# Performance work log

Hardware: AMD Instinct MI355X
Metric: run time of the kernel (lower is better)

## Reference

```python
import jax, jax.numpy as jnp
import numpy as np

EPS = 1e-5

def _layernorm(x, g, b):
    mu = jnp.mean(x, axis=-1, keepdims=True)
    var = jnp.mean(jnp.square(x - mu), axis=-1, keepdims=True)
    return (x - mu) * jax.lax.rsqrt(var + EPS) * g + b

def setup_inputs() -> dict:
    S, B, D, H, F = 4096, 2, 512, 8, 2048
    key = jax.random.key(0)
    ks = jax.random.split(key, 10)
    sc = 0.02
    return {
        "src": jax.random.normal(ks[0], (S, B, D), jnp.float32),
        "qkv_w": jax.random.normal(ks[1], (3 * D, D), jnp.float32) * sc,
        "qkv_b": jnp.zeros((3 * D,), jnp.float32),
        "out_w": jax.random.normal(ks[2], (D, D), jnp.float32) * sc,
        "w1": jax.random.normal(ks[3], (F, D), jnp.float32) * sc,
        "b1": jnp.zeros((F,), jnp.float32),
        "w2": jax.random.normal(ks[4], (D, F), jnp.float32) * sc,
        "b2": jnp.zeros((D,), jnp.float32),
        "ln1_g": jnp.ones((D,), jnp.float32),
        "ln1_b": jnp.zeros((D,), jnp.float32),
        "ln2_g": jnp.ones((D,), jnp.float32),
        "ln2_b": jnp.zeros((D,), jnp.float32),
    }

def reference(src, qkv_w, qkv_b, out_w, w1, b1, w2, b2, ln1_g, ln1_b, ln2_g, ln2_b):
    S, B, D = src.shape
    H = 8
    hd = D // H
    # --- self attention (NOTE: no 1/sqrt(hd) scaling, matching source) ---
    qkv = src @ qkv_w.T + qkv_b                      # [S, B, 3D]
    q, k, v = jnp.split(qkv, 3, axis=-1)             # each [S, B, D]
    # [S, B*H, hd] -> [B*H, S, hd]
    q = q.reshape(S, B * H, hd).transpose(1, 0, 2)
    k = k.reshape(S, B * H, hd).transpose(1, 0, 2)
    v = v.reshape(S, B * H, hd).transpose(1, 0, 2)
    scores = jnp.einsum('nqd,nkd->nqk', q, k)        # [B*H, S, S]
    attn = jax.nn.softmax(scores, axis=-1)           # dropout = identity (eval)
    out = jnp.einsum('nqk,nkd->nqd', attn, v)        # [B*H, S, hd]
    out = out.transpose(1, 0, 2).reshape(S, B, D)
    attn_out = out @ out_w.T                         # out_proj has no bias
    # --- post-norm residual + FFN ---
    x = _layernorm(src + attn_out, ln1_g, ln1_b)
    ffn = jax.nn.relu(x @ w1.T + b1) @ w2.T + b2
    x = _layernorm(x + ffn, ln2_g, ln2_b)
    return x
```

## Files before the change

### kernel.cpp

```cpp
#include <hip/hip_runtime.h>
#include <cstdint>
#include <math.h>

#define CF4(p) (*reinterpret_cast<const float4*>(p))
#define F4(p)  (*reinterpret_cast<float4*>(p))

typedef __attribute__((ext_vector_type(8))) short bf16x8;
typedef __attribute__((ext_vector_type(4))) float f32x4;

__device__ __forceinline__ unsigned short f2bf(float x) {
  union { float f; unsigned int u; } v; v.f = x;
  unsigned int r = v.u + 0x7FFF + ((v.u >> 16) & 1);
  return (unsigned short)(r >> 16);
}

__device__ __forceinline__ int swz(int row, int col) {
  return row * 64 + (col ^ ((row & 7) << 3));
}

__device__ __forceinline__ void gload_lds16(const void* g, void* lds) {
  __builtin_amdgcn_global_load_lds(
      (const __attribute__((address_space(1))) void*)g,
      (__attribute__((address_space(3))) void*)lds, 16, 0, 0);
}

__global__ __launch_bounds__(256) void cvt_kernel(
    unsigned short* __restrict__ dst, const float* __restrict__ s, int n8)
{
  const int i = blockIdx.x * 256 + threadIdx.x;
  if (i >= n8) return;
  float4 a = CF4(&s[i * 8]), b = CF4(&s[i * 8 + 4]);
  union { bf16x8 v; unsigned short u[8]; } w;
  w.u[0] = f2bf(a.x); w.u[1] = f2bf(a.y); w.u[2] = f2bf(a.z); w.u[3] = f2bf(a.w);
  w.u[4] = f2bf(b.x); w.u[5] = f2bf(b.y); w.u[6] = f2bf(b.z); w.u[7] = f2bf(b.w);
  *reinterpret_cast<bf16x8*>(&dst[i * 8]) = w.v;
}

template<int BIAS, int RELU, int RES, int OBF>
__global__ __launch_bounds__(256, 2) void bgemm_kernel(
    void* __restrict__ Cv, const unsigned short* __restrict__ A,
    const unsigned short* __restrict__ W, const float* __restrict__ bias,
    const float* __restrict__ R, int M, int N, int K)
{
  __shared__ __align__(16) unsigned short As[2][128 * 64];
  __shared__ __align__(16) unsigned short Ws[2][128 * 64];

  const int t    = threadIdx.x;
  const int lane = t & 63, wid = t >> 6;
  const int g    = lane >> 4, lr = lane & 15;
  const int wm   = wid >> 1,  wn = wid & 1;
  const int m0   = blockIdx.y * 128, n0 = blockIdx.x * 128;

  const int sr8 = lane >> 3;
  const int sc  = (lane & 7) ^ sr8;
  const unsigned short* Ag = A + (size_t)(m0 + sr8) * K + sc * 8;
  const unsigned short* Wg = W + (size_t)(n0 + sr8) * K + sc * 8;

  f32x4 acc[4][4];
#pragma unroll
  for (int mi = 0; mi < 4; ++mi)
#pragma unroll
    for (int nj = 0; nj < 4; ++nj)
      acc[mi][nj] = (f32x4){0.f, 0.f, 0.f, 0.f};

#define STAGE_G(buf, k0)                                              \
  {                                                                   \
    _Pragma("unroll")                                                 \
    for (int i = 0; i < 4; ++i) {                                     \
      const int rb = wid * 32 + i * 8;                                \
      gload_lds16(Ag + (size_t)rb * K + (k0), (void*)&As[buf][rb * 64]); \
      gload_lds16(Wg + (size_t)rb * K + (k0), (void*)&Ws[buf][rb * 64]); \
    }                                                                 \
  }

  STAGE_G(0, 0);
  __syncthreads();

  const int nk = K >> 6;
  for (int kt = 0; kt < nk; ++kt) {
    const int cur = kt & 1;
    if (kt + 1 < nk) STAGE_G(cur ^ 1, (kt + 1) * 64);
#pragma unroll
    for (int ks = 0; ks < 2; ++ks) {
      bf16x8 af[4], bfr[4];
#pragma unroll
      for (int mi = 0; mi < 4; ++mi) {
        const int row = wm * 64 + mi * 16 + lr;
        af[mi] = *reinterpret_cast<const bf16x8*>(
            &As[cur][row * 64 + (((ks * 4 + g) ^ (row & 7)) * 8)]);
      }
#pragma unroll
      for (int nj = 0; nj < 4; ++nj) {
        const int row = wn * 64 + nj * 16 + lr;
        bfr[nj] = *reinterpret_cast<const bf16x8*>(
            &Ws[cur][row * 64 + (((ks * 4 + g) ^ (row & 7)) * 8)]);
      }
#pragma unroll
      for (int mi = 0; mi < 4; ++mi)
#pragma unroll
        for (int nj = 0; nj < 4; ++nj)
          acc[mi][nj] = __builtin_amdgcn_mfma_f32_16x16x32_bf16(
              af[mi], bfr[nj], acc[mi][nj], 0, 0, 0);
    }
    __syncthreads();
  }
#undef STAGE_G

#pragma unroll
  for (int mi = 0; mi < 4; ++mi) {
#pragma unroll
    for (int reg = 0; reg < 4; ++reg) {
      const int r = m0 + wm * 64 + mi * 16 + g * 4 + reg;
#pragma unroll
      for (int nj = 0; nj < 4; ++nj) {
        const int cc = n0 + wn * 64 + nj * 16 + lr;
        float v = acc[mi][nj][reg];
        if (BIAS) v += bias[cc];
        if (RES)  v += R[(size_t)r * N + cc];
        if (RELU) v = fmaxf(v, 0.f);
        if (OBF)  ((unsigned short*)Cv)[(size_t)r * N + cc] = f2bf(v);
        else      ((float*)Cv)[(size_t)r * N + cc] = v;
      }
    }
  }
}

__global__ __launch_bounds__(256, 2) void attn_kernel(
    unsigned short* __restrict__ O, const unsigned short* __restrict__ qkv)
{
  const int Bb = 2, LD = 1536, DM = 512;
  const int qt = blockIdx.x;
  const int nh = blockIdx.y;
  const int b = nh >> 3, h = nh & 7;
  const int cq = h * 64, ck = 512 + h * 64, cv = 1024 + h * 64;

  __shared__ __align__(16) unsigned short Ks [2][64 * 64];
  __shared__ __align__(16) unsigned short Vts[2][64 * 64];
  __shared__ __align__(16) unsigned short Ps [128 * 64];

  const int t    = threadIdx.x;
  const int lane = t & 63;
  const int wid  = t >> 6;
  const int g    = lane >> 4;
  const int lr   = lane & 15;
  const int wq0  = wid * 32;

  bf16x8 qf[2][2];
#pragma unroll
  for (int mi = 0; mi < 2; ++mi)
#pragma unroll
    for (int kq = 0; kq < 2; ++kq)
      qf[mi][kq] = *reinterpret_cast<const bf16x8*>(
          &qkv[((size_t)(qt * 128 + wq0 + mi * 16 + lr) * Bb + b) * LD
               + cq + kq * 32 + g * 8]);

  f32x4 o_acc[2][4];
  float lsum[2] = {0.f, 0.f};
#pragma unroll
  for (int mi = 0; mi < 2; ++mi)
#pragma unroll
    for (int dj = 0; dj < 4; ++dj)
      o_acc[mi][dj] = (f32x4){0.f, 0.f, 0.f, 0.f};

  const int sr8 = lane >> 3;
  const int scK = (lane & 7) ^ sr8;
  const int vD0 = wid * 8;
  const int vSr = lane;

#define STAGE_K(buf, kt)                                               \
  {                                                                    \
    _Pragma("unroll")                                                  \
    for (int i = 0; i < 2; ++i) {                                      \
      const int rb = wid * 16 + i * 8;                                 \
      gload_lds16(&qkv[((size_t)((kt) * 64 + rb + sr8) * Bb + b) * LD  \
                       + ck + scK * 8],                                \
                  (void*)&Ks[buf][rb * 64]);                           \
    }                                                                  \
  }
#define LOAD_V(kt)                                                     \
  {                                                                    \
    _Pragma("unroll")                                                  \
    for (int p = 0; p < 2; ++p)                                        \
      vr[p] = *reinterpret_cast<const bf16x8*>(                        \
          &qkv[((size_t)((kt) * 64 + vSr) * Bb + b) * LD + cv          \
               + vD0 + p * 32]);                                       \
  }
#define WRITE_V(buf)                                                   \
  {                                                                    \
    _Pragma("unroll")                                                  \
    for (int p = 0; p < 2; ++p) {                                      \
      const int d0 = vD0 + p * 32;                                     \
      union { bf16x8 v; unsigned short u[8]; } w;                      \
      w.v = vr[p];                                                     \
      _Pragma("unroll")                                                \
      for (int j = 0; j < 8; ++j)                                      \
        Vts[buf][swz(d0 + j, vSr)] = w.u[j];                           \
    }                                                                  \
  }

  bf16x8 vr[2];
  STAGE_K(0, 0);
  LOAD_V(0);
  WRITE_V(0);
  __syncthreads();

  for (int kt = 0; kt < 64; ++kt) {
    const int cur = kt & 1;
    const bool hasNext = (kt < 63);
    if (hasNext) { STAGE_K(cur ^ 1, kt + 1); LOAD_V(kt + 1); }

    f32x4 sfT[2][4];
#pragma unroll
    for (int mi = 0; mi < 2; ++mi)
#pragma unroll
      for (int nj = 0; nj < 4; ++nj)
        sfT[mi][nj] = (f32x4){0.f, 0.f, 0.f, 0.f};
    __builtin_amdgcn_s_setprio(1);
#pragma unroll
    for (int nj = 0; nj < 4; ++nj) {
#pragma unroll
      for (int kq = 0; kq < 2; ++kq) {
        bf16x8 ak = *reinterpret_cast<const bf16x8*>(
            &Ks[cur][swz(nj * 16 + lr, kq * 32 + g * 8)]);
        sfT[0][nj] = __builtin_amdgcn_mfma_f32_16x16x32_bf16(
            ak, qf[0][kq], sfT[0][nj], 0, 0, 0);
        sfT[1][nj] = __builtin_amdgcn_mfma_f32_16x16x32_bf16(
            ak, qf[1][kq], sfT[1][nj], 0, 0, 0);
      }
    }
    __builtin_amdgcn_s_setprio(0);

#pragma unroll
    for (int mi = 0; mi < 2; ++mi) {
      const int qrow = wq0 + mi * 16 + lr;
#pragma unroll
      for (int nj = 0; nj < 4; ++nj) {
        const float p0 = __expf(sfT[mi][nj][0]);
        const float p1 = __expf(sfT[mi][nj][1]);
        const float p2 = __expf(sfT[mi][nj][2]);
        const float p3 = __expf(sfT[mi][nj][3]);
        lsum[mi] += (p0 + p1) + (p2 + p3);
        unsigned int w0, w1;
        asm("v_cvt_pk_bf16_f32 %0, %1, %2" : "=v"(w0) : "v"(p0), "v"(p1));
        asm("v_cvt_pk_bf16_f32 %0, %1, %2" : "=v"(w1) : "v"(p2), "v"(p3));
        *reinterpret_cast<uint2*>(&Ps[swz(qrow, nj * 16 + g * 4)]) =
            make_uint2(w0, w1);
      }
    }

    __builtin_amdgcn_s_setprio(1);
#pragma unroll
    for (int kks = 0; kks < 2; ++kks) {
      bf16x8 pa0 = *reinterpret_cast<const bf16x8*>(
          &Ps[swz(wq0 +  0 + lr, kks * 32 + g * 8)]);
      bf16x8 pa1 = *reinterpret_cast<const bf16x8*>(
          &Ps[swz(wq0 + 16 + lr, kks * 32 + g * 8)]);
#pragma unroll
      for (int dj = 0; dj < 4; ++dj) {
        bf16x8 vb = *reinterpret_cast<const bf16x8*>(
            &Vts[cur][swz(dj * 16 + lr, kks * 32 + g * 8)]);
        o_acc[0][dj] = __builtin_amdgcn_mfma_f32_16x16x32_bf16(
            pa0, vb, o_acc[0][dj], 0, 0, 0);
        o_acc[1][dj] = __builtin_amdgcn_mfma_f32_16x16x32_bf16(
            pa1, vb, o_acc[1][dj], 0, 0, 0);
      }
    }
    __builtin_amdgcn_s_setprio(0);

    if (hasNext) WRITE_V(cur ^ 1);
    __syncthreads();
  }
#undef STAGE_K
#undef LOAD_V
#undef WRITE_V

#pragma unroll
  for (int mi = 0; mi < 2; ++mi) {
    float rs = lsum[mi];
    rs += __shfl_xor(rs, 16);
    rs += __shfl_xor(rs, 32);
#pragma unroll
    for (int reg = 0; reg < 4; ++reg) {
      const float rsq = __shfl(rs, (lane & 48) + g * 4 + reg);
      const float inv = 1.f / rsq;
      const int q = qt * 128 + wq0 + mi * 16 + g * 4 + reg;
#pragma unroll
      for (int dj = 0; dj < 4; ++dj)
        O[((size_t)q * Bb + b) * DM + h * 64 + dj * 16 + lr] =
            f2bf(o_acc[mi][dj][reg] * inv);
    }
  }
}

template<int WBF>
__global__ __launch_bounds__(256) void ln_kernel(
    float* __restrict__ out, unsigned short* __restrict__ obf,
    const float* __restrict__ in, const float* __restrict__ g,
    const float* __restrict__ bb)
{
  const int w = threadIdx.x >> 6, lane = threadIdx.x & 63;
  const size_t row = (size_t)blockIdx.x * 4 + w;
  const float* xr = in + row * 512;
  float4 v0 = CF4(&xr[lane * 4]);
  float4 v1 = CF4(&xr[256 + lane * 4]);
  float s = v0.x + v0.y + v0.z + v0.w + v1.x + v1.y + v1.z + v1.w;
  float q = v0.x*v0.x + v0.y*v0.y + v0.z*v0.z + v0.w*v0.w
          + v1.x*v1.x + v1.y*v1.y + v1.z*v1.z + v1.w*v1.w;
#pragma unroll
  for (int off = 1; off < 64; off <<= 1) {
    s += __shfl_xor(s, off);
    q += __shfl_xor(q, off);
  }
  const float mu  = s * (1.f / 512.f);
  const float var = q * (1.f / 512.f) - mu * mu;
  const float rst = rsqrtf(var + 1e-5f);
  float4 g0 = CF4(&g[lane * 4]),  g1 = CF4(&g[256 + lane * 4]);
  float4 b0 = CF4(&bb[lane * 4]), b1 = CF4(&bb[256 + lane * 4]);
  float* orow = out + row * 512;
  float4 o0, o1;
  o0.x = (v0.x - mu) * rst * g0.x + b0.x;
  o0.y = (v0.y - mu) * rst * g0.y + b0.y;
  o0.z = (v0.z - mu) * rst * g0.z + b0.z;
  o0.w = (v0.w - mu) * rst * g0.w + b0.w;
  o1.x = (v1.x - mu) * rst * g1.x + b1.x;
  o1.y = (v1.y - mu) * rst * g1.y + b1.y;
  o1.z = (v1.z - mu) * rst * g1.z + b1.z;
  o1.w = (v1.w - mu) * rst * g1.w + b1.w;
  F4(&orow[lane * 4]) = o0;
  F4(&orow[256 + lane * 4]) = o1;
  if (WBF) {
    unsigned short* brow = obf + row * 512;
    ushort4 u0 = make_ushort4(f2bf(o0.x), f2bf(o0.y), f2bf(o0.z), f2bf(o0.w));
    ushort4 u1 = make_ushort4(f2bf(o1.x), f2bf(o1.y), f2bf(o1.z), f2bf(o1.w));
    *reinterpret_cast<ushort4*>(&brow[lane * 4]) = u0;
    *reinterpret_cast<ushort4*>(&brow[256 + lane * 4]) = u1;
  }
}

extern "C" void kernel_launch(void* const* d_in, const int* in_sizes, int n_in,
                              void* d_out, int out_size, void* d_ws, size_t ws_size,
                              hipStream_t stream)
{
  const float* src   = (const float*)d_in[0];
  const float* qkv_w = (const float*)d_in[1];
  const float* qkv_b = (const float*)d_in[2];
  const float* out_w = (const float*)d_in[3];
  const float* w1    = (const float*)d_in[4];
  const float* b1    = (const float*)d_in[5];
  const float* w2    = (const float*)d_in[6];
  const float* b2    = (const float*)d_in[7];
  const float* ln1g  = (const float*)d_in[8];
  const float* ln1b  = (const float*)d_in[9];
  const float* ln2g  = (const float*)d_in[10];
  const float* ln2b  = (const float*)d_in[11];
  float* out = (float*)d_out;

  const int M = 8192;

  char* ws = (char*)d_ws;
  unsigned short* qkv_bf  = (unsigned short*)(ws + 0);
  unsigned short* attn_bf = (unsigned short*)(ws + 25165824);
  unsigned short* h_bf    = (unsigned short*)(ws + 0);
  float*          y       = (float*)(ws + 33554432);
  float*          z       = (float*)(ws + 33554432);
  float*          x       = (float*)(ws + 50331648);
  unsigned short* x_bf    = (unsigned short*)(ws + 67108864);
  unsigned short* src_bf  = (unsigned short*)(ws + 75497472);
  unsigned short* wqkv_bf = (unsigned short*)(ws + 83886080);
  unsigned short* wout_bf = (unsigned short*)(ws + 85458944);
  unsigned short* w1_bf   = (unsigned short*)(ws + 85983232);
  unsigned short* w2_bf   = (unsigned short*)(ws + 88080384);
  if (ws_size < (size_t)90177536) return;

  dim3 blk(256);

  cvt_kernel<<<dim3(2048), blk, 0, stream>>>(src_bf, src, 524288);
  cvt_kernel<<<dim3(384),  blk, 0, stream>>>(wqkv_bf, qkv_w, 98304);
  cvt_kernel<<<dim3(128),  blk, 0, stream>>>(wout_bf, out_w, 32768);
  cvt_kernel<<<dim3(512),  blk, 0, stream>>>(w1_bf, w1, 131072);
  cvt_kernel<<<dim3(512),  blk, 0, stream>>>(w2_bf, w2, 131072);

  bgemm_kernel<1,0,0,1><<<dim3(12, 64), blk, 0, stream>>>(
      qkv_bf, src_bf, wqkv_bf, qkv_b, nullptr, M, 1536, 512);
  attn_kernel<<<dim3(32, 16), blk, 0, stream>>>(attn_bf, qkv_bf);
  bgemm_kernel<0,0,1,0><<<dim3(4, 64), blk, 0, stream>>>(
      y, attn_bf, wout_bf, nullptr, src, M, 512, 512);
  ln_kernel<1><<<dim3(M / 4), blk, 0, stream>>>(x, x_bf, y, ln1g, ln1b);
  bgemm_kernel<1,1,0,1><<<dim3(16, 64), blk, 0, stream>>>(
      h_bf, x_bf, w1_bf, b1, nullptr, M, 2048, 512);
  bgemm_kernel<1,0,1,0><<<dim3(4, 64), blk, 0, stream>>>(
      z, h_bf, w2_bf, b2, x, M, 512, 2048);
  ln_kernel<0><<<dim3(M / 4), blk, 0, stream>>>(out, nullptr, z, ln2g, ln2b);
}
```

Before: 321.7 us.

## Merge weight conversions, narrow N tiles for D=512 GEMMs, enlarge attention blocks

Merges the five fp32-to-bf16 conversion launches into a single kernel. Adds a template parameter for the GEMM N tile and uses 64-wide tiles for the two N=512 GEMMs, doubling their grid to 512 blocks for better CU fill. The attention kernel moves to 512 threads covering 256 queries per block, with K/V staging split over 8 waves so each K/V tile is reused by more queries. Risks: lower per-block arithmetic intensity in the narrow GEMMs, and in attention fewer blocks (256) plus more LDS and register pressure per block.

```diff
diff --git a/kernel.cpp b/kernel.cpp
--- a/kernel.cpp
+++ b/kernel.cpp
@@ -24,53 +24,68 @@
       (__attribute__((address_space(3))) void*)lds, 16, 0, 0);
 }
 
-__global__ __launch_bounds__(256) void cvt_kernel(
-    unsigned short* __restrict__ dst, const float* __restrict__ s, int n8)
-{
-  const int i = blockIdx.x * 256 + threadIdx.x;
-  if (i >= n8) return;
+__global__ __launch_bounds__(256) void cvt_all_kernel(
+    const float* __restrict__ src,   unsigned short* __restrict__ src_bf,
+    const float* __restrict__ qkvw,  unsigned short* __restrict__ qkvw_bf,
+    const float* __restrict__ outw,  unsigned short* __restrict__ outw_bf,
+    const float* __restrict__ w1,    unsigned short* __restrict__ w1_bf,
+    const float* __restrict__ w2,    unsigned short* __restrict__ w2_bf)
+{
+  int i = blockIdx.x * 256 + threadIdx.x;
+  const float* s; unsigned short* d;
+  if      (i < 524288) { s = src;  d = src_bf;                        }
+  else if (i < 622592) { s = qkvw; d = qkvw_bf; i -= 524288;          }
+  else if (i < 655360) { s = outw; d = outw_bf; i -= 622592;          }
+  else if (i < 786432) { s = w1;   d = w1_bf;   i -= 655360;          }
+  else if (i < 917504) { s = w2;   d = w2_bf;   i -= 786432;          }
+  else return;
   float4 a = CF4(&s[i * 8]), b = CF4(&s[i * 8 + 4]);
   union { bf16x8 v; unsigned short u[8]; } w;
   w.u[0] = f2bf(a.x); w.u[1] = f2bf(a.y); w.u[2] = f2bf(a.z); w.u[3] = f2bf(a.w);
   w.u[4] = f2bf(b.x); w.u[5] = f2bf(b.y); w.u[6] = f2bf(b.z); w.u[7] = f2bf(b.w);
-  *reinterpret_cast<bf16x8*>(&dst[i * 8]) = w.v;
-}
-
-template<int BIAS, int RELU, int RES, int OBF>
+  *reinterpret_cast<bf16x8*>(&d[i * 8]) = w.v;
+}
+
+template<int BNT, int BIAS, int RELU, int RES, int OBF>
 __global__ __launch_bounds__(256, 2) void bgemm_kernel(
     void* __restrict__ Cv, const unsigned short* __restrict__ A,
     const unsigned short* __restrict__ W, const float* __restrict__ bias,
     const float* __restrict__ R, int M, int N, int K)
 {
+  constexpr int NJ = BNT / 32;
   __shared__ __align__(16) unsigned short As[2][128 * 64];
-  __shared__ __align__(16) unsigned short Ws[2][128 * 64];
+  __shared__ __align__(16) unsigned short Ws[2][BNT * 64];
 
   const int t    = threadIdx.x;
   const int lane = t & 63, wid = t >> 6;
   const int g    = lane >> 4, lr = lane & 15;
   const int wm   = wid >> 1,  wn = wid & 1;
-  const int m0   = blockIdx.y * 128, n0 = blockIdx.x * 128;
+  const int m0   = blockIdx.y * 128, n0 = blockIdx.x * BNT;
 
   const int sr8 = lane >> 3;
   const int sc  = (lane & 7) ^ sr8;
   const unsigned short* Ag = A + (size_t)(m0 + sr8) * K + sc * 8;
   const unsigned short* Wg = W + (size_t)(n0 + sr8) * K + sc * 8;
 
-  f32x4 acc[4][4];
+  f32x4 acc[4][NJ];
 #pragma unroll
   for (int mi = 0; mi < 4; ++mi)
 #pragma unroll
-    for (int nj = 0; nj < 4; ++nj)
+    for (int nj = 0; nj < NJ; ++nj)
       acc[mi][nj] = (f32x4){0.f, 0.f, 0.f, 0.f};
 
-#define STAGE_G(buf, k0)                                              \
-  {                                                                   \
-    _Pragma("unroll")                                                 \
-    for (int i = 0; i < 4; ++i) {                                     \
-      const int rb = wid * 32 + i * 8;                                \
-      gload_lds16(Ag + (size_t)rb * K + (k0), (void*)&As[buf][rb * 64]); \
-      gload_lds16(Wg + (size_t)rb * K + (k0), (void*)&Ws[buf][rb * 64]); \
-    }                                                                 \
+#define STAGE_G(buf, k0)                                                   \
+  {                                                                        \
+    _Pragma("unroll")                                                      \
+    for (int i = 0; i < 4; ++i) {                                          \
+      const int rb = wid * 32 + i * 8;                                     \
+      gload_lds16(Ag + (size_t)rb * K + (k0), (void*)&As[buf][rb * 64]);   \
+    }                                                                      \
+    _Pragma("unroll")                                                      \
+    for (int i = 0; i < BNT / 32; ++i) {                                   \
+      const int rb = wid * (BNT / 4) + i * 8;                              \
+      gload_lds16(Wg + (size_t)rb * K + (k0), (void*)&Ws[buf][rb * 64]);   \
+    }                                                                      \
   }
 
   STAGE_G(0, 0);
@@ -82,7 +97,7 @@
     if (kt + 1 < nk) STAGE_G(cur ^ 1, (kt + 1) * 64);
 #pragma unroll
     for (int ks = 0; ks < 2; ++ks) {
-      bf16x8 af[4], bfr[4];
+      bf16x8 af[4], bfr[NJ];
 #pragma unroll
       for (int mi = 0; mi < 4; ++mi) {
         const int row = wm * 64 + mi * 16 + lr;
@@ -90,15 +105,15 @@
             &As[cur][row * 64 + (((ks * 4 + g) ^ (row & 7)) * 8)]);
       }
 #pragma unroll
-      for (int nj = 0; nj < 4; ++nj) {
-        const int row = wn * 64 + nj * 16 + lr;
+      for (int nj = 0; nj < NJ; ++nj) {
+        const int row = wn * (BNT / 2) + nj * 16 + lr;
         bfr[nj] = *reinterpret_cast<const bf16x8*>(
             &Ws[cur][row * 64 + (((ks * 4 + g) ^ (row & 7)) * 8)]);
       }
 #pragma unroll
       for (int mi = 0; mi < 4; ++mi)
 #pragma unroll
-        for (int nj = 0; nj < 4; ++nj)
+        for (int nj = 0; nj < NJ; ++nj)
           acc[mi][nj] = __builtin_amdgcn_mfma_f32_16x16x32_bf16(
               af[mi], bfr[nj], acc[mi][nj], 0, 0, 0);
     }
@@ -112,8 +127,8 @@
     for (int reg = 0; reg < 4; ++reg) {
       const int r = m0 + wm * 64 + mi * 16 + g * 4 + reg;
 #pragma unroll
-      for (int nj = 0; nj < 4; ++nj) {
-        const int cc = n0 + wn * 64 + nj * 16 + lr;
+      for (int nj = 0; nj < NJ; ++nj) {
+        const int cc = n0 + wn * (BNT / 2) + nj * 16 + lr;
         float v = acc[mi][nj][reg];
         if (BIAS) v += bias[cc];
         if (RES)  v += R[(size_t)r * N + cc];
@@ -125,7 +140,7 @@
   }
 }
 
-__global__ __launch_bounds__(256, 2) void attn_kernel(
+__global__ __launch_bounds__(512, 2) void attn_kernel(
     unsigned short* __restrict__ O, const unsigned short* __restrict__ qkv)
 {
   const int Bb = 2, LD = 1536, DM = 512;
@@ -136,7 +151,7 @@
 
   __shared__ __align__(16) unsigned short Ks [2][64 * 64];
   __shared__ __align__(16) unsigned short Vts[2][64 * 64];
-  __shared__ __align__(16) unsigned short Ps [128 * 64];
+  __shared__ __align__(16) unsigned short Ps [256 * 64];
 
   const int t    = threadIdx.x;
   const int lane = t & 63;
@@ -151,7 +166,7 @@
 #pragma unroll
     for (int kq = 0; kq < 2; ++kq)
       qf[mi][kq] = *reinterpret_cast<const bf16x8*>(
-          &qkv[((size_t)(qt * 128 + wq0 + mi * 16 + lr) * Bb + b) * LD
+          &qkv[((size_t)(qt * 256 + wq0 + mi * 16 + lr) * Bb + b) * LD
                + cq + kq * 32 + g * 8]);
 
   f32x4 o_acc[2][4];
@@ -169,36 +184,26 @@
 
 #define STAGE_K(buf, kt)                                               \
   {                                                                    \
-    _Pragma("unroll")                                                  \
-    for (int i = 0; i < 2; ++i) {                                      \
-      const int rb = wid * 16 + i * 8;                                 \
-      gload_lds16(&qkv[((size_t)((kt) * 64 + rb + sr8) * Bb + b) * LD  \
-                       + ck + scK * 8],                                \
-                  (void*)&Ks[buf][rb * 64]);                           \
-    }                                                                  \
+    const int rb = wid * 8;                                            \
+    gload_lds16(&qkv[((size_t)((kt) * 64 + rb + sr8) * Bb + b) * LD    \
+                     + ck + scK * 8],                                  \
+                (void*)&Ks[buf][rb * 64]);                             \
   }
 #define LOAD_V(kt)                                                     \
   {                                                                    \
-    _Pragma("unroll")                                                  \
-    for (int p = 0; p < 2; ++p)                                        \
-      vr[p] = *reinterpret_cast<const bf16x8*>(                        \
-          &qkv[((size_t)((kt) * 64 + vSr) * Bb + b) * LD + cv          \
-               + vD0 + p * 32]);                                       \
+    vr = *reinterpret_cast<const bf16x8*>(                             \
+        &qkv[((size_t)((kt) * 64 + vSr) * Bb + b) * LD + cv + vD0]);   \
   }
 #define WRITE_V(buf)                                                   \
   {                                                                    \
+    union { bf16x8 v; unsigned short u[8]; } w;                        \
+    w.v = vr;                                                          \
     _Pragma("unroll")                                                  \
-    for (int p = 0; p < 2; ++p) {                                      \
-      const int d0 = vD0 + p * 32;                                     \
-      union { bf16x8 v; unsigned short u[8]; } w;                      \
-      w.v = vr[p];                                                     \
-      _Pragma("unroll")                                                \
-      for (int j = 0; j < 8; ++j)                                      \
-        Vts[buf][swz(d0 + j, vSr)] = w.u[j];                           \
-    }                                                                  \
-  }
-
-  bf16x8 vr[2];
+    for (int j = 0; j < 8; ++j)                                        \
+      Vts[buf][swz(vD0 + j, vSr)] = w.u[j];                            \
+  }
+
+  bf16x8 vr;
   STAGE_K(0, 0);
   LOAD_V(0);
   WRITE_V(0);
@@ -283,7 +288,7 @@
     for (int reg = 0; reg < 4; ++reg) {
       const float rsq = __shfl(rs, (lane & 48) + g * 4 + reg);
       const float inv = 1.f / rsq;
-      const int q = qt * 128 + wq0 + mi * 16 + g * 4 + reg;
+      const int q = qt * 256 + wq0 + mi * 16 + g * 4 + reg;
 #pragma unroll
       for (int dj = 0; dj < 4; ++dj)
         O[((size_t)q * Bb + b) * DM + h * 64 + dj * 16 + lr] =
@@ -374,21 +379,18 @@
 
   dim3 blk(256);
 
-  cvt_kernel<<<dim3(2048), blk, 0, stream>>>(src_bf, src, 524288);
-  cvt_kernel<<<dim3(384),  blk, 0, stream>>>(wqkv_bf, qkv_w, 98304);
-  cvt_kernel<<<dim3(128),  blk, 0, stream>>>(wout_bf, out_w, 32768);
-  cvt_kernel<<<dim3(512),  blk, 0, stream>>>(w1_bf, w1, 131072);
-  cvt_kernel<<<dim3(512),  blk, 0, stream>>>(w2_bf, w2, 131072);
-
-  bgemm_kernel<1,0,0,1><<<dim3(12, 64), blk, 0, stream>>>(
+  cvt_all_kernel<<<dim3(3584), blk, 0, stream>>>(
+      src, src_bf, qkv_w, wqkv_bf, out_w, wout_bf, w1, w1_bf, w2, w2_bf);
+
+  bgemm_kernel<128,1,0,0,1><<<dim3(12, 64), blk, 0, stream>>>(
       qkv_bf, src_bf, wqkv_bf, qkv_b, nullptr, M, 1536, 512);
-  attn_kernel<<<dim3(32, 16), blk, 0, stream>>>(attn_bf, qkv_bf);
-  bgemm_kernel<0,0,1,0><<<dim3(4, 64), blk, 0, stream>>>(
+  attn_kernel<<<dim3(16, 16), dim3(512), 0, stream>>>(attn_bf, qkv_bf);
+  bgemm_kernel<64,0,0,1,0><<<dim3(8, 64), blk, 0, stream>>>(
       y, attn_bf, wout_bf, nullptr, src, M, 512, 512);
   ln_kernel<1><<<dim3(M / 4), blk, 0, stream>>>(x, x_bf, y, ln1g, ln1b);
-  bgemm_kernel<1,1,0,1><<<dim3(16, 64), blk, 0, stream>>>(
+  bgemm_kernel<128,1,1,0,1><<<dim3(16, 64), blk, 0, stream>>>(
       h_bf, x_bf, w1_bf, b1, nullptr, M, 2048, 512);
-  bgemm_kernel<1,0,1,0><<<dim3(4, 64), blk, 0, stream>>>(
+  bgemm_kernel<64,1,0,1,0><<<dim3(8, 64), blk, 0, stream>>>(
       z, h_bf, w2_bf, b2, x, M, 512, 2048);
   ln_kernel<0><<<dim3(M / 4), blk, 0, stream>>>(out, nullptr, z, ln2g, ln2b);
 }
```

Result: slower. 330.1 us (+2.6%).
